# Kernel tuning notes

Hardware: AMD Instinct MI355X
Metric: run time of the kernel (lower is better)

Reference implementation:

```python
import jax, jax.numpy as jnp
import numpy as np

N, F_DIM, H, K, T = 4096, 256, 256, 3, 5
START, END = 10, 3  # args.len_numerical_features, args.num_class


def setup_inputs() -> dict:
    key = jax.random.key(0)
    ks = jax.random.split(key, 8)
    s = 0.05
    x = jax.random.normal(ks[0], (N, F_DIM), dtype=jnp.float32)
    adj = jax.random.randint(ks[1], (N, N, K), 0, 2, dtype=jnp.int32)
    gnn_w = jax.random.normal(ks[2], (K, F_DIM, H), dtype=jnp.float32) * s
    gnn_b = jnp.zeros((K, H), dtype=jnp.float32)
    w_ih = jax.random.normal(ks[3], (K, 4 * H, H), dtype=jnp.float32) * s
    w_hh = jax.random.normal(ks[4], (K, 4 * H, H), dtype=jnp.float32) * s
    b_ih = jnp.zeros((K, 4 * H), dtype=jnp.float32)
    b_hh = jnp.zeros((K, 4 * H), dtype=jnp.float32)
    fc_w = jax.random.normal(ks[5], (K, F_DIM, H), dtype=jnp.float32) * s
    fc_b = jnp.zeros((K, F_DIM), dtype=jnp.float32)
    return dict(x=x, gnn_w=gnn_w, gnn_b=gnn_b, w_ih=w_ih, w_hh=w_hh,
                b_ih=b_ih, b_hh=b_hh, fc_w=fc_w, fc_b=fc_b, adj=adj)


def _gcn(x, a_bin, w, b):
    # PyG GCNConv: A_hat = A + I (self-loops added on top of existing edges,
    # weight 1), out = D^-1/2 A_hat D^-1/2 (x @ W) + b
    a = a_bin + jnp.eye(N, dtype=x.dtype)
    deg = a.sum(axis=1)
    dinv = jnp.where(deg > 0, jax.lax.rsqrt(deg), 0.0)
    a_norm = dinv[:, None] * a * dinv[None, :]
    return a_norm @ (x @ w) + b


def _lstm_last(xt, w_ih, w_hh, b_ih, b_hh):
    # batch_first LSTM over T identical inputs xt [N,H]; returns h at last step
    def step(carry, _):
        h, c = carry
        g = xt @ w_ih.T + b_ih + h @ w_hh.T + b_hh
        i, f, gg, o = jnp.split(g, 4, axis=-1)  # torch gate order: i, f, g, o
        c = jax.nn.sigmoid(f) * c + jax.nn.sigmoid(i) * jnp.tanh(gg)
        h = jax.nn.sigmoid(o) * jnp.tanh(c)
        return (h, c), None
    zero = jnp.zeros((xt.shape[0], H), dtype=xt.dtype)
    (h, c), _ = jax.lax.scan(step, (zero, zero), None, length=T)
    return h


def _sig_slice(z):
    return z.at[:, START:F_DIM - END].set(jax.nn.sigmoid(z[:, START:F_DIM - END]))


def reference(x, gnn_w, gnn_b, w_ih, w_hh, b_ih, b_hh, fc_w, fc_b, adj):
    deltas, zbars = [], []
    for k in range(K):
        a_bin = (adj[:, :, k] != 0).astype(x.dtype)
        # GCN output is identical across timesteps -> compute once
        gnn_out = _gcn(x, a_bin, gnn_w[k], gnn_b[k])
        h_last = _lstm_last(gnn_out, w_ih[k], w_hh[k], b_ih[k], b_hh[k])
        delta = jnp.tanh(h_last @ fc_w[k].T + fc_b[k])  # [N, F]
        deltas.append(delta)
        zbars.append(_sig_slice(x + delta))
    delta_z = jnp.stack(deltas, -1).mean(-1)
    res_z_bar = jnp.stack(zbars, -1)  # [N, F, K]
    pred_matrix = _sig_slice(x + delta_z)
    return pred_matrix, res_z_bar, adj
```

## Files before the change

### kernel.cpp

```cpp
#include <hip/hip_runtime.h>
#include <stdint.h>

#define NN_ 4096
#define FD 256
#define HD 256
#define KC 3
#define GD 1024
#define SA 40
#define PAG 40

typedef __attribute__((ext_vector_type(4))) unsigned int vu4;
typedef __attribute__((ext_vector_type(4))) int vi4;
typedef __attribute__((ext_vector_type(4))) float vf4;
typedef __attribute__((ext_vector_type(4))) unsigned short vus4;
typedef __attribute__((ext_vector_type(8))) short short8;
typedef __attribute__((ext_vector_type(4))) float f32x4;

__device__ __forceinline__ float b2f(unsigned short u) {
    unsigned int v = ((unsigned int)u) << 16; float f; __builtin_memcpy(&f, &v, 4); return f;
}
__device__ __forceinline__ unsigned short f2b(float x) {
    unsigned int u; __builtin_memcpy(&u, &x, 4);
    u = (u + 0x7FFFu + ((u >> 16) & 1u)) >> 16;
    return (unsigned short)u;
}
__device__ __forceinline__ void cvt8(const float* __restrict__ g, unsigned short* o) {
    vf4 a = *(const vf4*)g, b = *(const vf4*)(g + 4);
    o[0] = f2b(a[0]); o[1] = f2b(a[1]); o[2] = f2b(a[2]); o[3] = f2b(a[3]);
    o[4] = f2b(b[0]); o[5] = f2b(b[1]); o[6] = f2b(b[2]); o[7] = f2b(b[3]);
}
__device__ __forceinline__ float sigm(float v) { return 1.f / (1.f + __expf(-v)); }

__global__ __launch_bounds__(256) void adj_pass(const int* __restrict__ adj,
        float* __restrict__ adj_out, unsigned short* __restrict__ abk,
        float* __restrict__ dinv) {
    const int i = blockIdx.x, t = threadIdx.x;
    const int* src = adj + (size_t)i * 12288;
    float* dstf = adj_out + (size_t)i * 12288;
    float s0 = 0.f, s1 = 0.f, s2 = 0.f;
#pragma unroll
    for (int it = 0; it < 4; ++it) {
        int jq = (it * 256 + t) * 4;
        vi4 a = *(const vi4*)(src + jq * 3);
        vi4 b = *(const vi4*)(src + jq * 3 + 4);
        vi4 c = *(const vi4*)(src + jq * 3 + 8);
        int vv[12] = {a[0],a[1],a[2],a[3],b[0],b[1],b[2],b[3],c[0],c[1],c[2],c[3]};
        float ff[12];
#pragma unroll
        for (int e = 0; e < 12; ++e) ff[e] = vv[e] ? 1.f : 0.f;
        vf4 w0 = {ff[0],ff[1],ff[2],ff[3]}, w1 = {ff[4],ff[5],ff[6],ff[7]}, w2 = {ff[8],ff[9],ff[10],ff[11]};
        *(vf4*)(dstf + jq * 3) = w0; *(vf4*)(dstf + jq * 3 + 4) = w1; *(vf4*)(dstf + jq * 3 + 8) = w2;
#pragma unroll
        for (int k = 0; k < 3; ++k) {
            vus4 w;
            w[0] = vv[k]     ? (unsigned short)0x3F80 : (unsigned short)0;
            w[1] = vv[3 + k] ? (unsigned short)0x3F80 : (unsigned short)0;
            w[2] = vv[6 + k] ? (unsigned short)0x3F80 : (unsigned short)0;
            w[3] = vv[9 + k] ? (unsigned short)0x3F80 : (unsigned short)0;
            *(vus4*)(abk + ((size_t)(k * NN_ + i)) * NN_ + jq) = w;
        }
        s0 += ff[0] + ff[3] + ff[6] + ff[9];
        s1 += ff[1] + ff[4] + ff[7] + ff[10];
        s2 += ff[2] + ff[5] + ff[8] + ff[11];
    }
    __shared__ float r0[256], r1[256], r2[256];
    r0[t] = s0; r1[t] = s1; r2[t] = s2;
    __syncthreads();
    for (int off = 128; off > 0; off >>= 1) {
        if (t < off) { r0[t] += r0[t + off]; r1[t] += r1[t + off]; r2[t] += r2[t + off]; }
        __syncthreads();
    }
    if (t == 0) {
        dinv[i]            = 1.f / sqrtf(1.f + r0[0]);
        dinv[NN_ + i]      = 1.f / sqrtf(1.f + r1[0]);
        dinv[2 * NN_ + i]  = 1.f / sqrtf(1.f + r2[0]);
    }
}

__global__ __launch_bounds__(256) void wcvt(const float* __restrict__ wih,
        const float* __restrict__ whh, const float* __restrict__ fcw,
        unsigned short* __restrict__ wb) {
    size_t e = ((size_t)blockIdx.x * 256 + threadIdx.x) * 8;
    const float* src; size_t off;
    if (e < 786432)       { src = wih; off = e; }
    else if (e < 1572864) { src = whh; off = e - 786432; }
    else                  { src = fcw; off = e - 1572864; }
    alignas(16) unsigned short o[8];
    cvt8(src + off, o);
    *(vu4*)(wb + e) = *(vu4*)o;
}

__global__ __launch_bounds__(256) void gemm_xw(const float* __restrict__ x,
        const float* __restrict__ gw, const float* __restrict__ dinv,
        unsigned short* __restrict__ yT) {
    __shared__ __align__(16) unsigned short sA[64 * SA], sB[64 * SA];
    const int bi = blockIdx.x, bj = blockIdx.y, k = blockIdx.z;
    const int t = threadIdx.x, lane = t & 63, wave = t >> 6;
    const int m = lane & 15, q = lane >> 4, ko = q * 8;
    const int h0 = bj * 64;
    f32x4 acc[4] = {};
    const float* A0 = x + (size_t)(bi * 64) * FD;
    const float* B0 = gw + (size_t)k * FD * HD;
    const int r = t >> 2, c8 = (t & 3) << 3;
    const int fB = t >> 3, c8B = (t & 7) << 3;
    for (int k0 = 0; k0 < FD; k0 += 32) {
        alignas(16) unsigned short tA[8], tB[8];
        cvt8(A0 + (size_t)r * FD + k0 + c8, tA);
        *(vu4*)(sA + r * SA + c8) = *(vu4*)tA;
        cvt8(B0 + (size_t)(k0 + fB) * HD + h0 + c8B, tB);
#pragma unroll
        for (int e = 0; e < 8; ++e) sB[(c8B + e) * SA + fB] = tB[e];
        __syncthreads();
        short8 af = *(const short8*)(sA + (wave * 16 + m) * SA + ko);
#pragma unroll
        for (int ct = 0; ct < 4; ++ct) {
            short8 bf = *(const short8*)(sB + (ct * 16 + m) * SA + ko);
            acc[ct] = __builtin_amdgcn_mfma_f32_16x16x32_bf16(af, bf, acc[ct], 0, 0, 0);
        }
        __syncthreads();
    }
    unsigned short* yTk = yT + (size_t)k * HD * NN_;
#pragma unroll
    for (int ct = 0; ct < 4; ++ct)
#pragma unroll
        for (int r2 = 0; r2 < 4; ++r2) {
            int col = h0 + ct * 16 + m;
            int row = bi * 64 + wave * 16 + q * 4 + r2;
            yTk[(size_t)col * NN_ + row] = f2b(acc[ct][r2] * dinv[(size_t)k * NN_ + row]);
        }
}

__global__ __launch_bounds__(256) void gemm_agg(const unsigned short* __restrict__ abk,
        const unsigned short* __restrict__ yT, unsigned short* __restrict__ pbuf) {
    __shared__ __align__(16) unsigned short sA[128 * PAG], sB[128 * PAG];
    const int bh = blockIdx.x, bi = blockIdx.y, z = blockIdx.z;
    const int k = z >> 2, s = z & 3;
    const int t = threadIdx.x, lane = t & 63, wave = t >> 6;
    const int wi = wave & 1, wh = wave >> 1;
    const int m = lane & 15, q = lane >> 4, ko = q * 8;
    const int i0 = bi * 128, h0 = bh * 128, jbase = s * 1024;
    f32x4 acc[4][4] = {};
    const int r = t >> 1, cS = (t & 1) << 4;
    const unsigned short* Ab = abk + ((size_t)(k * NN_ + i0 + r)) * NN_ + jbase + cS;
    const unsigned short* Bb = yT + ((size_t)(k * 256 + h0 + r)) * NN_ + jbase + cS;
    for (int j0 = 0; j0 < 1024; j0 += 32) {
        *(vu4*)(sA + r * PAG + cS)     = *(const vu4*)(Ab + j0);
        *(vu4*)(sA + r * PAG + cS + 8) = *(const vu4*)(Ab + j0 + 8);
        *(vu4*)(sB + r * PAG + cS)     = *(const vu4*)(Bb + j0);
        *(vu4*)(sB + r * PAG + cS + 8) = *(const vu4*)(Bb + j0 + 8);
        __syncthreads();
        short8 af[4], bf[4];
#pragma unroll
        for (int rt = 0; rt < 4; ++rt)
            af[rt] = *(const short8*)(sA + (wi * 64 + rt * 16 + m) * PAG + ko);
#pragma unroll
        for (int ct = 0; ct < 4; ++ct)
            bf[ct] = *(const short8*)(sB + (wh * 64 + ct * 16 + m) * PAG + ko);
#pragma unroll
        for (int ct = 0; ct < 4; ++ct)
#pragma unroll
            for (int rt = 0; rt < 4; ++rt)
                acc[rt][ct] = __builtin_amdgcn_mfma_f32_16x16x32_bf16(af[rt], bf[ct], acc[rt][ct], 0, 0, 0);
        __syncthreads();
    }
    const int addself = ((bi >> 3) == s);
#pragma unroll
    for (int rt = 0; rt < 4; ++rt)
#pragma unroll
        for (int ct = 0; ct < 4; ++ct)
#pragma unroll
            for (int r2 = 0; r2 < 4; ++r2) {
                int row = i0 + wi * 64 + rt * 16 + q * 4 + r2;
                int col = h0 + wh * 64 + ct * 16 + m;
                float v = acc[rt][ct][r2];
                if (addself) v += b2f(yT[((size_t)k * 256 + col) * NN_ + row]);
                pbuf[(((size_t)s * 3 + k) * NN_ + row) * 256 + col] = f2b(v);
            }
}

__global__ __launch_bounds__(256) void agg_reduce(const unsigned short* __restrict__ pbuf,
        const float* __restrict__ dinv, const float* __restrict__ gnnb,
        unsigned short* __restrict__ xt) {
    size_t e8 = ((size_t)blockIdx.x * 256 + threadIdx.x) * 8;
    int k = (int)(e8 >> 20);
    int i = (int)((e8 >> 8) & 4095);
    int h = (int)(e8 & 255);
    float di = dinv[k * NN_ + i];
    const size_t KIH = (size_t)KC * NN_ * HD;
    alignas(16) unsigned short p0[8], p1[8], p2[8], p3[8], o[8];
    *(vu4*)p0 = *(const vu4*)(pbuf + 0 * KIH + e8);
    *(vu4*)p1 = *(const vu4*)(pbuf + 1 * KIH + e8);
    *(vu4*)p2 = *(const vu4*)(pbuf + 2 * KIH + e8);
    *(vu4*)p3 = *(const vu4*)(pbuf + 3 * KIH + e8);
#pragma unroll
    for (int e = 0; e < 8; ++e) {
        float v = b2f(p0[e]) + b2f(p1[e]) + b2f(p2[e]) + b2f(p3[e]);
        o[e] = f2b(di * v + gnnb[k * HD + h + e]);
    }
    *(vu4*)(xt + e8) = *(vu4*)o;
}

__global__ __launch_bounds__(256) void lstm_mm(const unsigned short* __restrict__ A,
        const unsigned short* __restrict__ W, const float* __restrict__ b1,
        const float* __restrict__ b2, unsigned short* __restrict__ gX2,
        float* __restrict__ cbuf, unsigned short* __restrict__ hbuf, int mode) {
    __shared__ __align__(16) unsigned short sA[128 * SA];
    __shared__ __align__(16) unsigned short sB[4][32 * SA];
    const int chb = blockIdx.x, bn = blockIdx.y;
    const int t = threadIdx.x, lane = t & 63, wave = t >> 6;
    const int m = lane & 15, q = lane >> 4, ko = q * 8;
    const int kk = bn >> 5;
    f32x4 acc[2][2][4] = {};
    const unsigned short* A0 = A + (size_t)bn * 128 * 256;
    const unsigned short* W0 = W + (size_t)kk * GD * 256 + (size_t)chb * 32 * 256;
    const int r = t >> 1, cS = (t & 1) << 4;
    const int gB = r >> 5, chB = r & 31;
    for (int k0 = 0; k0 < 256; k0 += 32) {
        *(vu4*)(sA + r * SA + cS)     = *(const vu4*)(A0 + (size_t)r * 256 + k0 + cS);
        *(vu4*)(sA + r * SA + cS + 8) = *(const vu4*)(A0 + (size_t)r * 256 + k0 + cS + 8);
        const unsigned short* wsrc = W0 + (size_t)(gB * 256 + chB) * 256 + k0 + cS;
        *(vu4*)(&sB[gB][chB * SA + cS])     = *(const vu4*)wsrc;
        *(vu4*)(&sB[gB][chB * SA + cS + 8]) = *(const vu4*)(wsrc + 8);
        __syncthreads();
        short8 af[2];
#pragma unroll
        for (int rt = 0; rt < 2; ++rt)
            af[rt] = *(const short8*)(sA + (wave * 32 + rt * 16 + m) * SA + ko);
#pragma unroll
        for (int g = 0; g < 4; ++g)
#pragma unroll
            for (int cc = 0; cc < 2; ++cc) {
                short8 bf = *(const short8*)(&sB[g][(cc * 16 + m) * SA + ko]);
#pragma unroll
                for (int rt = 0; rt < 2; ++rt)
                    acc[rt][cc][g] = __builtin_amdgcn_mfma_f32_16x16x32_bf16(af[rt], bf, acc[rt][cc][g], 0, 0, 0);
            }
        __syncthreads();
    }
#pragma unroll
    for (int rt = 0; rt < 2; ++rt)
#pragma unroll
        for (int cc = 0; cc < 2; ++cc)
#pragma unroll
            for (int r2 = 0; r2 < 4; ++r2) {
                int row = bn * 128 + wave * 32 + rt * 16 + q * 4 + r2;
                int ch = chb * 32 + cc * 16 + m;
                size_t goff = ((size_t)row * 256 + ch) * 4;
                if (mode == 0) {
                    vus4 o;
#pragma unroll
                    for (int g = 0; g < 4; ++g) {
                        float v = acc[rt][cc][g][r2]
                                + b1[kk * GD + g * 256 + ch] + b2[kk * GD + g * 256 + ch];
                        o[g] = f2b(v);
                    }
                    *(vus4*)(gX2 + goff) = o;
                } else {
                    vus4 gv = *(const vus4*)(gX2 + goff);
                    float iv = acc[rt][cc][0][r2] + b2f(gv[0]);
                    float fv = acc[rt][cc][1][r2] + b2f(gv[1]);
                    float gg = acc[rt][cc][2][r2] + b2f(gv[2]);
                    float ov = acc[rt][cc][3][r2] + b2f(gv[3]);
                    size_t coff = (size_t)row * 256 + ch;
                    float cn = sigm(fv) * cbuf[coff] + sigm(iv) * tanhf(gg);
                    cbuf[coff] = cn;
                    hbuf[coff] = f2b(sigm(ov) * tanhf(cn));
                }
            }
}

__global__ __launch_bounds__(256) void lstm_cell0(const unsigned short* __restrict__ gX2,
        float* __restrict__ cbuf, unsigned short* __restrict__ hbuf) {
    size_t e8 = ((size_t)blockIdx.x * 256 + threadIdx.x) * 8;
    size_t gb = e8 * 4;
    alignas(16) unsigned short gx[32], h8[8];
    alignas(16) float cv[8];
#pragma unroll
    for (int v = 0; v < 4; ++v)
        *(vu4*)(gx + v * 8) = *(const vu4*)(gX2 + gb + v * 8);
#pragma unroll
    for (int e = 0; e < 8; ++e) {
        float iv = b2f(gx[e * 4 + 0]), gg = b2f(gx[e * 4 + 2]), ov = b2f(gx[e * 4 + 3]);
        float cn = sigm(iv) * tanhf(gg);
        cv[e] = cn;
        h8[e] = f2b(sigm(ov) * tanhf(cn));
    }
    *(vf4*)(cbuf + e8)     = *(vf4*)cv;
    *(vf4*)(cbuf + e8 + 4) = *(vf4*)(cv + 4);
    *(vu4*)(hbuf + e8) = *(vu4*)h8;
}

__global__ __launch_bounds__(256) void gemm_nt_ep(const unsigned short* __restrict__ A,
        const unsigned short* __restrict__ W, const float* __restrict__ b1,
        unsigned short* __restrict__ outp, int COLS, int do_tanh) {
    __shared__ __align__(16) unsigned short sA[64 * SA], sB[64 * SA];
    const int bg = blockIdx.x, bn = blockIdx.y, k = blockIdx.z;
    const int t = threadIdx.x, lane = t & 63, wave = t >> 6;
    const int m = lane & 15, q = lane >> 4, ko = q * 8;
    f32x4 acc[4] = {};
    const unsigned short* A0 = A + ((size_t)k * NN_ + bn * 64) * HD;
    const unsigned short* W0 = W + ((size_t)k * COLS + bg * 64) * HD;
    const int r = t >> 2, c8 = (t & 3) << 3;
    for (int k0 = 0; k0 < HD; k0 += 32) {
        *(vu4*)(sA + r * SA + c8) = *(const vu4*)(A0 + (size_t)r * HD + k0 + c8);
        *(vu4*)(sB + r * SA + c8) = *(const vu4*)(W0 + (size_t)r * HD + k0 + c8);
        __syncthreads();
        short8 af = *(const short8*)(sA + (wave * 16 + m) * SA + ko);
#pragma unroll
        for (int ct = 0; ct < 4; ++ct) {
            short8 bf = *(const short8*)(sB + (ct * 16 + m) * SA + ko);
            acc[ct] = __builtin_amdgcn_mfma_f32_16x16x32_bf16(af, bf, acc[ct], 0, 0, 0);
        }
        __syncthreads();
    }
#pragma unroll
    for (int ct = 0; ct < 4; ++ct)
#pragma unroll
        for (int r2 = 0; r2 < 4; ++r2) {
            int col = bg * 64 + ct * 16 + m;
            int row = bn * 64 + wave * 16 + q * 4 + r2;
            float v = acc[ct][r2];
            if (b1) v += b1[(size_t)k * COLS + col];
            if (do_tanh) v = tanhf(v);
            outp[((size_t)k * NN_ + row) * COLS + col] = f2b(v);
        }
}

__global__ __launch_bounds__(256) void final_ep(const float* __restrict__ x,
        const unsigned short* __restrict__ delta, float* __restrict__ pred,
        float* __restrict__ res) {
    int idx = blockIdx.x * 256 + threadIdx.x;
    size_t base = (size_t)idx * 8;
    int f0 = (int)(base & 255);
    alignas(16) unsigned short d0[8], d1[8], d2[8];
    alignas(16) float pr[8], rs[24];
    vf4 xa = *(const vf4*)(x + base), xb = *(const vf4*)(x + base + 4);
    float xs[8] = { xa[0], xa[1], xa[2], xa[3], xb[0], xb[1], xb[2], xb[3] };
    *(vu4*)d0 = *(const vu4*)(delta + base);
    *(vu4*)d1 = *(const vu4*)(delta + (size_t)NN_ * FD + base);
    *(vu4*)d2 = *(const vu4*)(delta + 2 * (size_t)NN_ * FD + base);
#pragma unroll
    for (int e = 0; e < 8; ++e) {
        int f = f0 + e;
        bool sg = (f >= 10) && (f < 253);
        float xf = xs[e];
        float da = b2f(d0[e]), db = b2f(d1[e]), dc = b2f(d2[e]);
        float dm = (da + db + dc) * (1.f / 3.f);
        float p = xf + dm; if (sg) p = sigm(p);
        pr[e] = p;
        float z0 = xf + da; if (sg) z0 = sigm(z0);
        float z1 = xf + db; if (sg) z1 = sigm(z1);
        float z2 = xf + dc; if (sg) z2 = sigm(z2);
        rs[e * 3 + 0] = z0; rs[e * 3 + 1] = z1; rs[e * 3 + 2] = z2;
    }
    *(vf4*)(pred + base)     = *(vf4*)pr;
    *(vf4*)(pred + base + 4) = *(vf4*)(pr + 4);
    size_t rb = base * 3;
#pragma unroll
    for (int v = 0; v < 6; ++v)
        *(vf4*)(res + rb + v * 4) = *(vf4*)(rs + v * 4);
}

extern "C" void kernel_launch(void* const* d_in, const int* in_sizes, int n_in,
                              void* d_out, int out_size, void* d_ws, size_t ws_size,
                              hipStream_t stream) {
    const float* x    = (const float*)d_in[0];
    const float* gnnw = (const float*)d_in[1];
    const float* gnnb = (const float*)d_in[2];
    const float* wih  = (const float*)d_in[3];
    const float* whh  = (const float*)d_in[4];
    const float* bih  = (const float*)d_in[5];
    const float* bhh  = (const float*)d_in[6];
    const float* fcw  = (const float*)d_in[7];
    const float* fcb  = (const float*)d_in[8];
    const int*   adj  = (const int*)d_in[9];

    float* out = (float*)d_out;
    float* out_pred = out;
    float* out_res  = out + (size_t)NN_ * FD;
    float* out_adj  = out + (size_t)NN_ * FD * 4;

    char* ws = (char*)d_ws;
    float*          dinv  = (float*)ws;
    unsigned short* R1    = (unsigned short*)(ws + 49152);
    unsigned short* R2    = (unsigned short*)(ws + 6340608);
    unsigned short* wb    = (unsigned short*)(ws + 12632064);
    unsigned short* pbuf  = (unsigned short*)(ws + 16171008);
    unsigned short* gX2   = pbuf;
    unsigned short* abk   = (unsigned short*)(ws + 41336832);
    float*          cbuf  = (float*)(ws + 142000128);
    const unsigned short* wihb = wb;
    const unsigned short* whhb = wb + 786432;
    const unsigned short* fcwb = wb + 1572864;
    (void)ws_size; (void)in_sizes; (void)n_in; (void)out_size;

    wcvt<<<dim3(864), 256, 0, stream>>>(wih, whh, fcw, wb);
    adj_pass<<<dim3(4096), 256, 0, stream>>>(adj, out_adj, abk, dinv);
    gemm_xw<<<dim3(64, 4, 3), 256, 0, stream>>>(x, gnnw, dinv, R1 );
    gemm_agg<<<dim3(2, 32, 12), 256, 0, stream>>>(abk, R1 , pbuf);
    agg_reduce<<<dim3(1536), 256, 0, stream>>>(pbuf, dinv, gnnb, R2 );
    lstm_mm<<<dim3(8, 96), 256, 0, stream>>>(R2 , wihb, bih, bhh, gX2, nullptr, nullptr, 0);
    lstm_cell0<<<dim3(1536), 256, 0, stream>>>(gX2, cbuf, R1 );
    for (int tstep = 1; tstep < 5; ++tstep)
        lstm_mm<<<dim3(8, 96), 256, 0, stream>>>(R1 , whhb, nullptr, nullptr, gX2, cbuf, R1 , 1);
    gemm_nt_ep<<<dim3(4, 64, 3), 256, 0, stream>>>(R1 , fcwb, fcb, R2 , FD, 1);
    final_ep<<<dim3(512), 256, 0, stream>>>(x, R2 , out_pred, out_res);
}
```

Measured before the change: 639.3 us.

## Load GEMM tiles directly into LDS and remap blocks for XCD locality

Replaces register-staged global-to-LDS copies in the aggregation, LSTM and FC GEMMs with global_load_lds direct DMA into unpadded 32-wide LDS tiles. Also flattens the gemm_agg and lstm_mm grids to 1D and permutes block IDs so that consecutive logical tiles land on the same XCD, aiming for better L2 reuse of shared operands. Dropping the padding may add LDS bank conflicts on the MFMA operand reads, and loads still are not double-buffered.

After: 622.3 us. -2.7%, faster.

```diff
diff --git a/kernel.cpp b/kernel.cpp
--- a/kernel.cpp
+++ b/kernel.cpp
@@ -7,7 +7,6 @@
 #define KC 3
 #define GD 1024
 #define SA 40
-#define PAG 40
 
 typedef __attribute__((ext_vector_type(4))) unsigned int vu4;
 typedef __attribute__((ext_vector_type(4))) int vi4;
@@ -15,6 +14,12 @@
 typedef __attribute__((ext_vector_type(4))) unsigned short vus4;
 typedef __attribute__((ext_vector_type(8))) short short8;
 typedef __attribute__((ext_vector_type(4))) float f32x4;
+
+typedef __attribute__((address_space(1))) const void GV;
+typedef __attribute__((address_space(3))) void LV;
+__device__ __forceinline__ void gl16(const void* g, void* l) {
+    __builtin_amdgcn_global_load_lds((GV*)g, (LV*)l, 16, 0, 0);
+}
 
 __device__ __forceinline__ float b2f(unsigned short u) {
     unsigned int v = ((unsigned int)u) << 16; float f; __builtin_memcpy(&f, &v, 4); return f;
@@ -132,30 +137,38 @@
 
 __global__ __launch_bounds__(256) void gemm_agg(const unsigned short* __restrict__ abk,
         const unsigned short* __restrict__ yT, unsigned short* __restrict__ pbuf) {
-    __shared__ __align__(16) unsigned short sA[128 * PAG], sB[128 * PAG];
-    const int bh = blockIdx.x, bi = blockIdx.y, z = blockIdx.z;
+    __shared__ __align__(16) unsigned short sA[128 * 32], sB[128 * 32];
+    const int d = blockIdx.x;
+    const int w = (d & 7) * 96 + (d >> 3);
+    const int bh = w & 1, bi = (w >> 1) & 31, z = w >> 6;
     const int k = z >> 2, s = z & 3;
     const int t = threadIdx.x, lane = t & 63, wave = t >> 6;
     const int wi = wave & 1, wh = wave >> 1;
     const int m = lane & 15, q = lane >> 4, ko = q * 8;
     const int i0 = bi * 128, h0 = bh * 128, jbase = s * 1024;
     f32x4 acc[4][4] = {};
-    const int r = t >> 1, cS = (t & 1) << 4;
-    const unsigned short* Ab = abk + ((size_t)(k * NN_ + i0 + r)) * NN_ + jbase + cS;
-    const unsigned short* Bb = yT + ((size_t)(k * 256 + h0 + r)) * NN_ + jbase + cS;
+    const int lrow = lane >> 2, lcol = (lane & 3) << 3;
+    const unsigned short* Ag0 = abk + ((size_t)(k * NN_ + i0 + wave * 32 + lrow)) * NN_ + jbase + lcol;
+    const unsigned short* Ag1 = Ag0 + (size_t)16 * NN_;
+    const unsigned short* Bg0 = yT + ((size_t)(k * 256 + h0 + wave * 32 + lrow)) * NN_ + jbase + lcol;
+    const unsigned short* Bg1 = Bg0 + (size_t)16 * NN_;
+    unsigned short* lA0 = sA + (wave * 32) * 32;
+    unsigned short* lA1 = lA0 + 16 * 32;
+    unsigned short* lB0 = sB + (wave * 32) * 32;
+    unsigned short* lB1 = lB0 + 16 * 32;
     for (int j0 = 0; j0 < 1024; j0 += 32) {
-        *(vu4*)(sA + r * PAG + cS)     = *(const vu4*)(Ab + j0);
-        *(vu4*)(sA + r * PAG + cS + 8) = *(const vu4*)(Ab + j0 + 8);
-        *(vu4*)(sB + r * PAG + cS)     = *(const vu4*)(Bb + j0);
-        *(vu4*)(sB + r * PAG + cS + 8) = *(const vu4*)(Bb + j0 + 8);
+        gl16(Ag0 + j0, lA0);
+        gl16(Ag1 + j0, lA1);
+        gl16(Bg0 + j0, lB0);
+        gl16(Bg1 + j0, lB1);
         __syncthreads();
         short8 af[4], bf[4];
 #pragma unroll
         for (int rt = 0; rt < 4; ++rt)
-            af[rt] = *(const short8*)(sA + (wi * 64 + rt * 16 + m) * PAG + ko);
+            af[rt] = *(const short8*)(sA + (wi * 64 + rt * 16 + m) * 32 + ko);
 #pragma unroll
         for (int ct = 0; ct < 4; ++ct)
-            bf[ct] = *(const short8*)(sB + (wh * 64 + ct * 16 + m) * PAG + ko);
+            bf[ct] = *(const short8*)(sB + (wh * 64 + ct * 16 + m) * 32 + ko);
 #pragma unroll
         for (int ct = 0; ct < 4; ++ct)
 #pragma unroll
@@ -204,33 +217,41 @@
         const unsigned short* __restrict__ W, const float* __restrict__ b1,
         const float* __restrict__ b2, unsigned short* __restrict__ gX2,
         float* __restrict__ cbuf, unsigned short* __restrict__ hbuf, int mode) {
-    __shared__ __align__(16) unsigned short sA[128 * SA];
-    __shared__ __align__(16) unsigned short sB[4][32 * SA];
-    const int chb = blockIdx.x, bn = blockIdx.y;
+    __shared__ __align__(16) unsigned short sA[128 * 32];
+    __shared__ __align__(16) unsigned short sB[128 * 32];
+    const int d = blockIdx.x;
+    const int w = (d & 7) * 96 + (d >> 3);
+    const int chb = w & 7, bn = w >> 3;
     const int t = threadIdx.x, lane = t & 63, wave = t >> 6;
     const int m = lane & 15, q = lane >> 4, ko = q * 8;
     const int kk = bn >> 5;
     f32x4 acc[2][2][4] = {};
+    const int lrow = lane >> 2, lcol = (lane & 3) << 3;
     const unsigned short* A0 = A + (size_t)bn * 128 * 256;
     const unsigned short* W0 = W + (size_t)kk * GD * 256 + (size_t)chb * 32 * 256;
-    const int r = t >> 1, cS = (t & 1) << 4;
-    const int gB = r >> 5, chB = r & 31;
+    const unsigned short* Ag0 = A0 + (size_t)(wave * 32 + lrow) * 256 + lcol;
+    const unsigned short* Ag1 = Ag0 + 16 * 256;
+    const unsigned short* Bg0 = W0 + (size_t)(wave * 256 + lrow) * 256 + lcol;
+    const unsigned short* Bg1 = Bg0 + 16 * 256;
+    unsigned short* lA0 = sA + (wave * 32) * 32;
+    unsigned short* lA1 = lA0 + 16 * 32;
+    unsigned short* lB0 = sB + (wave * 32) * 32;
+    unsigned short* lB1 = lB0 + 16 * 32;
     for (int k0 = 0; k0 < 256; k0 += 32) {
-        *(vu4*)(sA + r * SA + cS)     = *(const vu4*)(A0 + (size_t)r * 256 + k0 + cS);
-        *(vu4*)(sA + r * SA + cS + 8) = *(const vu4*)(A0 + (size_t)r * 256 + k0 + cS + 8);
-        const unsigned short* wsrc = W0 + (size_t)(gB * 256 + chB) * 256 + k0 + cS;
-        *(vu4*)(&sB[gB][chB * SA + cS])     = *(const vu4*)wsrc;
-        *(vu4*)(&sB[gB][chB * SA + cS + 8]) = *(const vu4*)(wsrc + 8);
+        gl16(Ag0 + k0, lA0);
+        gl16(Ag1 + k0, lA1);
+        gl16(Bg0 + k0, lB0);
+        gl16(Bg1 + k0, lB1);
         __syncthreads();
         short8 af[2];
 #pragma unroll
         for (int rt = 0; rt < 2; ++rt)
-            af[rt] = *(const short8*)(sA + (wave * 32 + rt * 16 + m) * SA + ko);
+            af[rt] = *(const short8*)(sA + (wave * 32 + rt * 16 + m) * 32 + ko);
 #pragma unroll
         for (int g = 0; g < 4; ++g)
 #pragma unroll
             for (int cc = 0; cc < 2; ++cc) {
-                short8 bf = *(const short8*)(&sB[g][(cc * 16 + m) * SA + ko]);
+                short8 bf = *(const short8*)(sB + (g * 32 + cc * 16 + m) * 32 + ko);
 #pragma unroll
                 for (int rt = 0; rt < 2; ++rt)
                     acc[rt][cc][g] = __builtin_amdgcn_mfma_f32_16x16x32_bf16(af[rt], bf, acc[rt][cc][g], 0, 0, 0);
@@ -293,22 +314,26 @@
 __global__ __launch_bounds__(256) void gemm_nt_ep(const unsigned short* __restrict__ A,
         const unsigned short* __restrict__ W, const float* __restrict__ b1,
         unsigned short* __restrict__ outp, int COLS, int do_tanh) {
-    __shared__ __align__(16) unsigned short sA[64 * SA], sB[64 * SA];
+    __shared__ __align__(16) unsigned short sA[64 * 32], sB[64 * 32];
     const int bg = blockIdx.x, bn = blockIdx.y, k = blockIdx.z;
     const int t = threadIdx.x, lane = t & 63, wave = t >> 6;
     const int m = lane & 15, q = lane >> 4, ko = q * 8;
     f32x4 acc[4] = {};
+    const int lrow = lane >> 2, lcol = (lane & 3) << 3;
     const unsigned short* A0 = A + ((size_t)k * NN_ + bn * 64) * HD;
     const unsigned short* W0 = W + ((size_t)k * COLS + bg * 64) * HD;
-    const int r = t >> 2, c8 = (t & 3) << 3;
+    const unsigned short* Ag = A0 + (size_t)(wave * 16 + lrow) * HD + lcol;
+    const unsigned short* Bg = W0 + (size_t)(wave * 16 + lrow) * HD + lcol;
+    unsigned short* lA = sA + (wave * 16) * 32;
+    unsigned short* lB = sB + (wave * 16) * 32;
     for (int k0 = 0; k0 < HD; k0 += 32) {
-        *(vu4*)(sA + r * SA + c8) = *(const vu4*)(A0 + (size_t)r * HD + k0 + c8);
-        *(vu4*)(sB + r * SA + c8) = *(const vu4*)(W0 + (size_t)r * HD + k0 + c8);
-        __syncthreads();
-        short8 af = *(const short8*)(sA + (wave * 16 + m) * SA + ko);
+        gl16(Ag + k0, lA);
+        gl16(Bg + k0, lB);
+        __syncthreads();
+        short8 af = *(const short8*)(sA + (wave * 16 + m) * 32 + ko);
 #pragma unroll
         for (int ct = 0; ct < 4; ++ct) {
-            short8 bf = *(const short8*)(sB + (ct * 16 + m) * SA + ko);
+            short8 bf = *(const short8*)(sB + (ct * 16 + m) * 32 + ko);
             acc[ct] = __builtin_amdgcn_mfma_f32_16x16x32_bf16(af, bf, acc[ct], 0, 0, 0);
         }
         __syncthreads();
@@ -397,12 +422,12 @@
     wcvt<<<dim3(864), 256, 0, stream>>>(wih, whh, fcw, wb);
     adj_pass<<<dim3(4096), 256, 0, stream>>>(adj, out_adj, abk, dinv);
     gemm_xw<<<dim3(64, 4, 3), 256, 0, stream>>>(x, gnnw, dinv, R1 );
-    gemm_agg<<<dim3(2, 32, 12), 256, 0, stream>>>(abk, R1 , pbuf);
+    gemm_agg<<<dim3(768), 256, 0, stream>>>(abk, R1 , pbuf);
     agg_reduce<<<dim3(1536), 256, 0, stream>>>(pbuf, dinv, gnnb, R2 );
-    lstm_mm<<<dim3(8, 96), 256, 0, stream>>>(R2 , wihb, bih, bhh, gX2, nullptr, nullptr, 0);
+    lstm_mm<<<dim3(768), 256, 0, stream>>>(R2 , wihb, bih, bhh, gX2, nullptr, nullptr, 0);
     lstm_cell0<<<dim3(1536), 256, 0, stream>>>(gX2, cbuf, R1 );
     for (int tstep = 1; tstep < 5; ++tstep)
-        lstm_mm<<<dim3(8, 96), 256, 0, stream>>>(R1 , whhb, nullptr, nullptr, gX2, cbuf, R1 , 1);
+        lstm_mm<<<dim3(768), 256, 0, stream>>>(R1 , whhb, nullptr, nullptr, gX2, cbuf, R1 , 1);
     gemm_nt_ep<<<dim3(4, 64, 3), 256, 0, stream>>>(R1 , fcwb, fcb, R2 , FD, 1);
     final_ep<<<dim3(512), 256, 0, stream>>>(x, R2 , out_pred, out_res);
 }
```
